# Performance work log

Measured on AMD Instinct MI355X. Metric: run time of the kernel, lower is better.

## Reference

```python
import jax, jax.numpy as jnp
import numpy as np

B, S, D = 4, 2048, 1024
NH, NKV = 16, 4
DK = D // NH          # 64
NG = NH // NKV        # 4


def _rope_tables(seq, d_k):
    theta = 1.0 / jnp.power(10000.0, jnp.arange(0, d_k, 2, dtype=jnp.float32) / d_k)
    ang = jnp.outer(jnp.arange(seq, dtype=jnp.float32), theta)  # [S, DK/2]
    ang = jnp.concatenate([ang, ang], axis=-1)                   # [S, DK]
    return jnp.cos(ang), jnp.sin(ang)


def _rotate_half(t):
    half = t.shape[-1] // 2
    return jnp.concatenate([-t[..., half:], t[..., :half]], axis=-1)


def _apply_rope(t, cos, sin):
    # t: [B, H, S, DK]; cos/sin: [S, DK]
    return t * cos + _rotate_half(t) * sin


def setup_inputs() -> dict:
    key = jax.random.key(0)
    ks = jax.random.split(key, 5)
    sc = 0.02
    x = jax.random.normal(ks[0], (B, S, D), dtype=jnp.float32)
    Wq = jax.random.normal(ks[1], (D, NH * DK), dtype=jnp.float32) * sc
    Wk = jax.random.normal(ks[2], (D, NKV * DK), dtype=jnp.float32) * sc
    Wv = jax.random.normal(ks[3], (D, NKV * DK), dtype=jnp.float32) * sc
    Wo = jax.random.normal(ks[4], (D, D), dtype=jnp.float32) * sc
    mask = jnp.tril(jnp.ones((S, S), dtype=bool))[None, None]  # causal [1,1,S,S]
    return {"x": x, "Wq": Wq, "Wk": Wk, "Wv": Wv, "Wo": Wo, "mask": mask}


def reference(x, Wq, Wk, Wv, Wo, mask):
    batch, seq, _ = x.shape
    q = (x @ Wq).reshape(batch, seq, NH, DK).transpose(0, 2, 1, 3)    # [B,NH,S,DK]
    k = (x @ Wk).reshape(batch, seq, NKV, DK).transpose(0, 2, 1, 3)   # [B,NKV,S,DK]
    v = (x @ Wv).reshape(batch, seq, NKV, DK).transpose(0, 2, 1, 3)

    cos, sin = _rope_tables(seq, DK)
    q = _apply_rope(q, cos, sin)
    k = _apply_rope(k, cos, sin)

    # GQA: repeat_interleave K/V along head dim
    k = jnp.repeat(k, NG, axis=1)  # [B,NH,S,DK]
    v = jnp.repeat(v, NG, axis=1)

    scores = jnp.einsum('bhqd,bhkd->bhqk', q, k) / jnp.sqrt(jnp.float32(DK))
    scores = jnp.where(mask, scores, jnp.float32(-jnp.inf))
    weights = jax.nn.softmax(scores, axis=-1)
    out = jnp.einsum('bhqk,bhkd->bhqd', weights, v)          # [B,NH,S,DK]
    out = out.transpose(0, 2, 1, 3).reshape(batch, seq, D)   # [B,S,D]
    return out @ Wo
```

## Files before the change

### kernel.cpp

```cpp
#include <hip/hip_runtime.h>

#define DEV __device__ __forceinline__

typedef short s16x8 __attribute__((ext_vector_type(8)));
typedef float f32x4 __attribute__((ext_vector_type(4)));


DEV unsigned short f2bf(float f) {
  union { float f; unsigned int u; } a; a.f = f;
  unsigned int u = a.u;
  u = (u + 0x7FFFu + ((u >> 16) & 1u)) >> 16;
  return (unsigned short)u;
}

DEV unsigned int bfpack2(float a, float b) {
  union { float f; unsigned int u; } x, y; x.f = a; y.f = b;
  return ((x.u + 0x8000u) >> 16) | ((y.u + 0x8000u) & 0xFFFF0000u);
}

DEV void gl_lds16(const void* g, void* l) {
  __builtin_amdgcn_global_load_lds(
      (const __attribute__((address_space(1))) unsigned int*)g,
      (__attribute__((address_space(3))) unsigned int*)l, 16, 0, 0);
}

__global__ __launch_bounds__(256) void cvt_kern(const float* __restrict__ src,
                                                unsigned short* __restrict__ dst) {
  int i = blockIdx.x * 256 + threadIdx.x;
  float4 v = ((const float4*)src)[i];
  ushort4 o = make_ushort4(f2bf(v.x), f2bf(v.y), f2bf(v.z), f2bf(v.w));
  ((ushort4*)dst)[i] = o;
}

__global__ __launch_bounds__(256) void transp_kern(const float* __restrict__ src,
                                                   unsigned short* __restrict__ dst,
                                                   int src_cols, int dst_off) {
  __shared__ float tile[32][33];
  int k0 = blockIdx.x * 32, n0 = blockIdx.y * 32;
  int tx = threadIdx.x & 31, ty = threadIdx.x >> 5;
  #pragma unroll
  for (int i = ty; i < 32; i += 8)
    tile[i][tx] = src[(k0 + i) * src_cols + (n0 + tx)];
  __syncthreads();
  #pragma unroll
  for (int i = ty; i < 32; i += 8)
    dst[(size_t)(n0 + i + dst_off) * 1024 + (k0 + tx)] = f2bf(tile[tx][i]);
}

template <int EPI>
__global__ __launch_bounds__(256) void gemm128(
    const unsigned short* __restrict__ A,
    const unsigned short* __restrict__ BT,
    unsigned short* __restrict__ Qbuf,
    unsigned short* __restrict__ Kbuf,
    unsigned short* __restrict__ VTbuf,
    float* __restrict__ Cout) {
  __shared__ __align__(16) unsigned short As[128 * 32];
  __shared__ __align__(16) unsigned short Bs[128 * 32];
  const int K = 1024;
  int m0 = blockIdx.x * 128, n0 = blockIdx.y * 128;
  int tid = threadIdx.x, w = tid >> 6, lane = tid & 63;
  int c4 = lane & 15, quad = lane >> 4;
  int m_off = (w & 1) * 64, n_off = (w >> 1) * 64;

  f32x4 acc[4][4];
  #pragma unroll
  for (int i = 0; i < 4; i++)
    #pragma unroll
    for (int j = 0; j < 4; j++) acc[i][j] = (f32x4){0.f, 0.f, 0.f, 0.f};

  int srow = (lane >> 2), sch = lane & 3;
  for (int kt = 0; kt < K / 32; ++kt) {
    int k0 = kt * 32;
    __syncthreads();
    #pragma unroll
    for (int ii = 0; ii < 2; ++ii) {
      int is = w * 2 + ii;
      int row = is * 16 + srow;
      gl_lds16(A + (size_t)(m0 + row) * K + k0 + sch * 8,
               (char*)As + is * 1024 + lane * 16);
      gl_lds16(BT + (size_t)(n0 + row) * K + k0 + sch * 8,
               (char*)Bs + is * 1024 + lane * 16);
    }
    __syncthreads();
    s16x8 a[4], b[4];
    #pragma unroll
    for (int mi = 0; mi < 4; ++mi)
      a[mi] = *(const s16x8*)((const char*)As + (m_off + mi * 16 + c4) * 64 + quad * 16);
    #pragma unroll
    for (int ni = 0; ni < 4; ++ni)
      b[ni] = *(const s16x8*)((const char*)Bs + (n_off + ni * 16 + c4) * 64 + quad * 16);
    #pragma unroll
    for (int mi = 0; mi < 4; ++mi)
      #pragma unroll
      for (int ni = 0; ni < 4; ++ni)
        acc[mi][ni] = __builtin_amdgcn_mfma_f32_16x16x32_bf16(a[mi], b[ni], acc[mi][ni], 0, 0, 0);
  }

  if (EPI == 1) {
    #pragma unroll
    for (int mi = 0; mi < 4; ++mi)
      #pragma unroll
      for (int ni = 0; ni < 4; ++ni)
        #pragma unroll
        for (int r = 0; r < 4; ++r) {
          int row = m0 + m_off + mi * 16 + quad * 4 + r;
          int col = n0 + n_off + ni * 16 + c4;
          Cout[(size_t)row * 1024 + col] = acc[mi][ni][r];
        }
  } else {
    int colbase = n0 + n_off;
    if (colbase < 1280) {
      const float CTH = 0.41524101186092029f;
      const float SC = 0.18033688011112042f;
      float th0 = exp2f(-(float)c4 * CTH);
      float th1 = exp2f(-(float)(c4 + 16) * CTH);
      bool isQ = colbase < 1024;
      float osc = isQ ? SC : 1.0f;
      #pragma unroll
      for (int mi = 0; mi < 4; ++mi)
        #pragma unroll
        for (int r = 0; r < 4; ++r) {
          int row = m0 + m_off + mi * 16 + quad * 4 + r;
          float pos = (float)(row & 2047);
          float a0 = pos * th0, a1 = pos * th1;
          float c0 = __cosf(a0), s0 = __sinf(a0);
          float c1 = __cosf(a1), s1 = __sinf(a1);
          float v0 = acc[mi][0][r], v1 = acc[mi][1][r];
          float v2 = acc[mi][2][r], v3 = acc[mi][3][r];
          float o0 = (v0 * c0 - v2 * s0) * osc;
          float o1 = (v1 * c1 - v3 * s1) * osc;
          float o2 = (v2 * c0 + v0 * s0) * osc;
          float o3 = (v3 * c1 + v1 * s1) * osc;
          if (isQ) {
            size_t base = (size_t)row * 1024 + colbase + c4;
            Qbuf[base] = f2bf(o0); Qbuf[base + 16] = f2bf(o1);
            Qbuf[base + 32] = f2bf(o2); Qbuf[base + 48] = f2bf(o3);
          } else {
            size_t base = (size_t)row * 256 + (colbase - 1024) + c4;
            Kbuf[base] = f2bf(o0); Kbuf[base + 16] = f2bf(o1);
            Kbuf[base + 32] = f2bf(o2); Kbuf[base + 48] = f2bf(o3);
          }
        }
    } else {
      #pragma unroll
      for (int mi = 0; mi < 4; ++mi)
        #pragma unroll
        for (int ni = 0; ni < 4; ++ni) {
          int row = m0 + m_off + mi * 16 + quad * 4;
          int c = colbase + ni * 16 + c4 - 1280;
          int bb = row >> 11, s = row & 2047;
          uint2 pv = make_uint2(bfpack2(acc[mi][ni][0], acc[mi][ni][1]),
                                bfpack2(acc[mi][ni][2], acc[mi][ni][3]));
          *(uint2*)(VTbuf + ((size_t)(bb * 256 + c)) * 2048 + s) = pv;
        }
    }
  }
}

__global__ __launch_bounds__(256, 4) void attn_kern(
    const unsigned short* __restrict__ Qbuf,
    const unsigned short* __restrict__ Kbuf,
    const unsigned short* __restrict__ VTbuf,
    unsigned short* __restrict__ Obuf) {
  __shared__ __align__(16) unsigned short Ks[2][64 * 64];
  __shared__ __align__(16) unsigned short VTs[2][64 * 64];
  __shared__ __align__(16) unsigned short Ps[4 * 16 * 64];

  int pr = blockIdx.x;
  int h = blockIdx.y, b = blockIdx.z, g = h >> 2;
  int tid = threadIdx.x, w = tid >> 6, lane = tid & 63;
  int c4 = lane & 15, quad = lane >> 4;
  int x7 = c4 & 7;
  unsigned short* Pw = Ps + w * 1024;

  int L0 = tid, L1 = tid + 256;
  int r0 = L0 >> 3, c0 = (L0 & 7) ^ (r0 & 7);
  int r1 = L1 >> 3, c1 = (L1 & 7) ^ (r1 & 7);
  const unsigned short* kB0 = Kbuf + (size_t)(b * 2048 + r0) * 256 + g * 64 + c0 * 8;
  const unsigned short* kB1 = Kbuf + (size_t)(b * 2048 + r1) * 256 + g * 64 + c1 * 8;
  const unsigned short* vB0 = VTbuf + (size_t)(b * 256 + g * 64 + r0) * 2048 + c0 * 8;
  const unsigned short* vB1 = VTbuf + (size_t)(b * 256 + g * 64 + r1) * 2048 + c1 * 8;

  for (int ph = 0; ph < 2; ++ph) {
    int qtile = ph ? (31 - pr) : pr;
    int nkv = qtile + 1;
    int q0 = qtile * 64;

    s16x8 bq[2];
    #pragma unroll
    for (int kk = 0; kk < 2; ++kk)
      bq[kk] = *(const s16x8*)(Qbuf +
          (size_t)(b * 2048 + q0 + w * 16 + c4) * 1024 + h * 64 + kk * 32 + quad * 8);

    const unsigned short* kS0 = kB0;
    const unsigned short* kS1 = kB1;
    const unsigned short* vS0 = vB0;
    const unsigned short* vS1 = vB1;

    f32x4 Oacc[4];
    #pragma unroll
    for (int nd = 0; nd < 4; ++nd) Oacc[nd] = (f32x4){0.f, 0.f, 0.f, 0.f};
    float m_st = -3e38f, l_st = 0.f;

    __syncthreads();
    gl_lds16(kS0, (char*)Ks[0] + L0 * 16);
    gl_lds16(kS1, (char*)Ks[0] + L1 * 16);
    gl_lds16(vS0, (char*)VTs[0] + L0 * 16);
    gl_lds16(vS1, (char*)VTs[0] + L1 * 16);
    kS0 += 64 * 256; kS1 += 64 * 256; vS0 += 64; vS1 += 64;

    for (int kt = 0; kt < nkv; ++kt) {
      int cur = kt & 1, nxt = cur ^ 1;
      __syncthreads();

      if (kt + 1 < nkv) {
        gl_lds16(kS0, (char*)Ks[nxt] + L0 * 16);
        gl_lds16(kS1, (char*)Ks[nxt] + L1 * 16);
        gl_lds16(vS0, (char*)VTs[nxt] + L0 * 16);
        gl_lds16(vS1, (char*)VTs[nxt] + L1 * 16);
        kS0 += 64 * 256; kS1 += 64 * 256; vS0 += 64; vS1 += 64;
      }

      const char* Kc = (const char*)Ks[cur];
      const char* Vc = (const char*)VTs[cur];

      f32x4 st[4];
      #pragma unroll
      for (int mt = 0; mt < 4; ++mt) st[mt] = (f32x4){0.f, 0.f, 0.f, 0.f};
      #pragma unroll
      for (int kk = 0; kk < 2; ++kk) {
        #pragma unroll
        for (int mt = 0; mt < 4; ++mt) {
          s16x8 ak = *(const s16x8*)(Kc + (mt * 16 + c4) * 128 +
                                     ((kk * 4 + quad) ^ x7) * 16);
          st[mt] = __builtin_amdgcn_mfma_f32_16x16x32_bf16(ak, bq[kk], st[mt], 0, 0, 0);
        }
      }

      int qmin = q0 + w * 16;
      if (kt * 64 + 63 > qmin) {
        int qi = qmin + c4;
        #pragma unroll
        for (int mt = 0; mt < 4; ++mt)
          #pragma unroll
          for (int r = 0; r < 4; ++r) {
            int kv = kt * 64 + mt * 16 + quad * 4 + r;
            if (kv > qi) st[mt][r] = -1e30f;
          }
      }

      float x0 = fmaxf(fmaxf(st[0][0], st[0][1]), fmaxf(st[0][2], st[0][3]));
      float x1 = fmaxf(fmaxf(st[1][0], st[1][1]), fmaxf(st[1][2], st[1][3]));
      float x2 = fmaxf(fmaxf(st[2][0], st[2][1]), fmaxf(st[2][2], st[2][3]));
      float x3 = fmaxf(fmaxf(st[3][0], st[3][1]), fmaxf(st[3][2], st[3][3]));
      float vmax = fmaxf(fmaxf(x0, x1), fmaxf(x2, x3));
      vmax = fmaxf(vmax, __shfl_xor(vmax, 16));
      vmax = fmaxf(vmax, __shfl_xor(vmax, 32));
      float mnew = fmaxf(m_st, vmax);
      float alpha = exp2f(m_st - mnew);
      m_st = mnew;

      #pragma unroll
      for (int mt = 0; mt < 4; ++mt)
        #pragma unroll
        for (int r = 0; r < 4; ++r) st[mt][r] = exp2f(st[mt][r] - mnew);
      float p0 = (st[0][0] + st[0][1]) + (st[0][2] + st[0][3]);
      float p1 = (st[1][0] + st[1][1]) + (st[1][2] + st[1][3]);
      float p2 = (st[2][0] + st[2][1]) + (st[2][2] + st[2][3]);
      float p3 = (st[3][0] + st[3][1]) + (st[3][2] + st[3][3]);
      float ssum = (p0 + p1) + (p2 + p3);
      ssum += __shfl_xor(ssum, 16);
      ssum += __shfl_xor(ssum, 32);
      l_st = l_st * alpha + ssum;

      #pragma unroll
      for (int nd = 0; nd < 4; ++nd)
        #pragma unroll
        for (int r = 0; r < 4; ++r) Oacc[nd][r] *= alpha;

      #pragma unroll
      for (int mt = 0; mt < 4; ++mt) {
        unsigned int lo = bfpack2(st[mt][0], st[mt][1]);
        unsigned int hi = bfpack2(st[mt][2], st[mt][3]);
        int cc = (mt * 2 + (quad >> 1)) ^ x7;
        *(uint2*)((char*)Pw + c4 * 128 + cc * 16 + (quad & 1) * 8) =
            make_uint2(lo, hi);
      }

      #pragma unroll
      for (int kk = 0; kk < 2; ++kk) {
        s16x8 ap = *(const s16x8*)((const char*)Pw + c4 * 128 +
                                   ((kk * 4 + quad) ^ x7) * 16);
        #pragma unroll
        for (int nd = 0; nd < 4; ++nd) {
          s16x8 av = *(const s16x8*)(Vc + (nd * 16 + c4) * 128 +
                                     ((kk * 4 + quad) ^ x7) * 16);
          Oacc[nd] = __builtin_amdgcn_mfma_f32_16x16x32_bf16(av, ap, Oacc[nd], 0, 0, 0);
        }
      }
    }

    float linv = 1.f / l_st;
    #pragma unroll
    for (int nd = 0; nd < 4; ++nd) {
      unsigned int lo = bfpack2(Oacc[nd][0] * linv, Oacc[nd][1] * linv);
      unsigned int hi = bfpack2(Oacc[nd][2] * linv, Oacc[nd][3] * linv);
      int cc = (nd * 2 + (quad >> 1)) ^ x7;
      *(uint2*)((char*)Pw + c4 * 128 + cc * 16 + (quad & 1) * 8) =
          make_uint2(lo, hi);
    }
    {
      int row = lane >> 2, j = lane & 3;
      int grow = b * 2048 + q0 + w * 16 + row;
      #pragma unroll
      for (int t = 0; t < 2; ++t) {
        int cb = j * 2 + t;
        uint4 v = *(const uint4*)((const char*)Pw + row * 128 +
                                  (cb ^ (row & 7)) * 16);
        *(uint4*)(Obuf + (size_t)grow * 1024 + h * 64 + cb * 8) = v;
      }
    }
  }
}

extern "C" void kernel_launch(void* const* d_in, const int* in_sizes, int n_in,
                              void* d_out, int out_size, void* d_ws, size_t ws_size,
                              hipStream_t stream) {
  const float* x  = (const float*)d_in[0];
  const float* Wq = (const float*)d_in[1];
  const float* Wk = (const float*)d_in[2];
  const float* Wv = (const float*)d_in[3];
  const float* Wo = (const float*)d_in[4];
  float* out = (float*)d_out;

  unsigned short* xb    = (unsigned short*)d_ws;
  unsigned short* WqkvT = xb + 8192 * 1024;
  unsigned short* WoT   = WqkvT + 1536 * 1024;
  unsigned short* Qbuf  = WoT + 1024 * 1024;
  unsigned short* Kbuf  = Qbuf + 8192 * 1024;
  unsigned short* VTbuf = Kbuf + 8192 * 256;
  unsigned short* Obuf  = VTbuf + 4 * 256 * 2048;

  cvt_kern<<<8192, 256, 0, stream>>>(x, xb);
  transp_kern<<<dim3(32, 32), 256, 0, stream>>>(Wq, WqkvT, 1024, 0);
  transp_kern<<<dim3(32, 8), 256, 0, stream>>>(Wk, WqkvT, 256, 1024);
  transp_kern<<<dim3(32, 8), 256, 0, stream>>>(Wv, WqkvT, 256, 1280);
  transp_kern<<<dim3(32, 32), 256, 0, stream>>>(Wo, WoT, 1024, 0);

  gemm128<0><<<dim3(64, 12), 256, 0, stream>>>(xb, WqkvT, Qbuf, Kbuf, VTbuf, nullptr);
  attn_kern<<<dim3(16, 16, 4), 256, 0, stream>>>(Qbuf, Kbuf, VTbuf, Obuf);
  gemm128<1><<<dim3(64, 8), 256, 0, stream>>>(Obuf, WoT, nullptr, nullptr, nullptr, out);
}
```

Baseline: 274.3 us.

## Widen GEMM K-tile to 64 with XOR-swizzled LDS, merge QKV transposes, truncate P

The bf16 GEMM now stages 64-wide K tiles into LDS with an XOR swizzle on 16-byte chunks. This halves the number of barrier-separated load iterations and is meant to avoid LDS bank conflicts on the fragment reads. The three Q/K/V weight transposes are merged into one launch. In attention, the probability packing switches from rounding to a single byte-permute truncation, trading a little precision for fewer ALU ops. LDS use doubles per GEMM block, which could reduce occupancy.

```diff
diff --git a/kernel.cpp b/kernel.cpp
--- a/kernel.cpp
+++ b/kernel.cpp
@@ -16,6 +16,11 @@
 DEV unsigned int bfpack2(float a, float b) {
   union { float f; unsigned int u; } x, y; x.f = a; y.f = b;
   return ((x.u + 0x8000u) >> 16) | ((y.u + 0x8000u) & 0xFFFF0000u);
+}
+
+DEV unsigned int pktrunc(float a, float b) {
+  union { float f; unsigned int u; } x, y; x.f = a; y.f = b;
+  return __builtin_amdgcn_perm(y.u, x.u, 0x07060302u);
 }
 
 DEV void gl_lds16(const void* g, void* l) {
@@ -45,6 +50,26 @@
   #pragma unroll
   for (int i = ty; i < 32; i += 8)
     dst[(size_t)(n0 + i + dst_off) * 1024 + (k0 + tx)] = f2bf(tile[tx][i]);
+}
+
+__global__ __launch_bounds__(256) void transp_qkv(const float* __restrict__ Wq,
+                                                  const float* __restrict__ Wk,
+                                                  const float* __restrict__ Wv,
+                                                  unsigned short* __restrict__ dst) {
+  __shared__ float tile[32][33];
+  int k0 = blockIdx.x * 32, n0 = blockIdx.y * 32;
+  const float* src; int sc, nloc;
+  if (n0 < 1024)      { src = Wq; sc = 1024; nloc = n0; }
+  else if (n0 < 1280) { src = Wk; sc = 256;  nloc = n0 - 1024; }
+  else                { src = Wv; sc = 256;  nloc = n0 - 1280; }
+  int tx = threadIdx.x & 31, ty = threadIdx.x >> 5;
+  #pragma unroll
+  for (int i = ty; i < 32; i += 8)
+    tile[i][tx] = src[(k0 + i) * sc + (nloc + tx)];
+  __syncthreads();
+  #pragma unroll
+  for (int i = ty; i < 32; i += 8)
+    dst[(size_t)(n0 + i) * 1024 + (k0 + tx)] = f2bf(tile[tx][i]);
 }
 
 template <int EPI>
@@ -55,12 +80,13 @@
     unsigned short* __restrict__ Kbuf,
     unsigned short* __restrict__ VTbuf,
     float* __restrict__ Cout) {
-  __shared__ __align__(16) unsigned short As[128 * 32];
-  __shared__ __align__(16) unsigned short Bs[128 * 32];
+  __shared__ __align__(16) unsigned short As[128 * 64];
+  __shared__ __align__(16) unsigned short Bs[128 * 64];
   const int K = 1024;
   int m0 = blockIdx.x * 128, n0 = blockIdx.y * 128;
   int tid = threadIdx.x, w = tid >> 6, lane = tid & 63;
   int c4 = lane & 15, quad = lane >> 4;
+  int x7 = c4 & 7;
   int m_off = (w & 1) * 64, n_off = (w >> 1) * 64;
 
   f32x4 acc[4][4];
@@ -69,32 +95,42 @@
     #pragma unroll
     for (int j = 0; j < 4; j++) acc[i][j] = (f32x4){0.f, 0.f, 0.f, 0.f};
 
-  int srow = (lane >> 2), sch = lane & 3;
-  for (int kt = 0; kt < K / 32; ++kt) {
-    int k0 = kt * 32;
+  const unsigned short* pA[4];
+  const unsigned short* pB[4];
+  #pragma unroll
+  for (int i = 0; i < 4; ++i) {
+    int slot = i * 256 + tid;
+    int row = slot >> 3, cs = slot & 7, lc = cs ^ (row & 7);
+    pA[i] = A + (size_t)(m0 + row) * K + lc * 8;
+    pB[i] = BT + (size_t)(n0 + row) * K + lc * 8;
+  }
+
+  for (int kt = 0; kt < K / 64; ++kt) {
     __syncthreads();
     #pragma unroll
-    for (int ii = 0; ii < 2; ++ii) {
-      int is = w * 2 + ii;
-      int row = is * 16 + srow;
-      gl_lds16(A + (size_t)(m0 + row) * K + k0 + sch * 8,
-               (char*)As + is * 1024 + lane * 16);
-      gl_lds16(BT + (size_t)(n0 + row) * K + k0 + sch * 8,
-               (char*)Bs + is * 1024 + lane * 16);
+    for (int i = 0; i < 4; ++i) {
+      int slot = i * 256 + tid;
+      gl_lds16(pA[i], (char*)As + slot * 16);
+      gl_lds16(pB[i], (char*)Bs + slot * 16);
+      pA[i] += 64; pB[i] += 64;
     }
     __syncthreads();
-    s16x8 a[4], b[4];
-    #pragma unroll
-    for (int mi = 0; mi < 4; ++mi)
-      a[mi] = *(const s16x8*)((const char*)As + (m_off + mi * 16 + c4) * 64 + quad * 16);
-    #pragma unroll
-    for (int ni = 0; ni < 4; ++ni)
-      b[ni] = *(const s16x8*)((const char*)Bs + (n_off + ni * 16 + c4) * 64 + quad * 16);
-    #pragma unroll
-    for (int mi = 0; mi < 4; ++mi)
+    #pragma unroll
+    for (int kk = 0; kk < 2; ++kk) {
+      s16x8 a[4], b[4];
+      int cc = ((kk * 4 + quad) ^ x7) * 16;
+      #pragma unroll
+      for (int mi = 0; mi < 4; ++mi)
+        a[mi] = *(const s16x8*)((const char*)As + (m_off + mi * 16 + c4) * 128 + cc);
       #pragma unroll
       for (int ni = 0; ni < 4; ++ni)
-        acc[mi][ni] = __builtin_amdgcn_mfma_f32_16x16x32_bf16(a[mi], b[ni], acc[mi][ni], 0, 0, 0);
+        b[ni] = *(const s16x8*)((const char*)Bs + (n_off + ni * 16 + c4) * 128 + cc);
+      #pragma unroll
+      for (int mi = 0; mi < 4; ++mi)
+        #pragma unroll
+        for (int ni = 0; ni < 4; ++ni)
+          acc[mi][ni] = __builtin_amdgcn_mfma_f32_16x16x32_bf16(a[mi], b[ni], acc[mi][ni], 0, 0, 0);
+    }
   }
 
   if (EPI == 1) {
@@ -281,8 +317,8 @@
 
       #pragma unroll
       for (int mt = 0; mt < 4; ++mt) {
-        unsigned int lo = bfpack2(st[mt][0], st[mt][1]);
-        unsigned int hi = bfpack2(st[mt][2], st[mt][3]);
+        unsigned int lo = pktrunc(st[mt][0], st[mt][1]);
+        unsigned int hi = pktrunc(st[mt][2], st[mt][3]);
         int cc = (mt * 2 + (quad >> 1)) ^ x7;
         *(uint2*)((char*)Pw + c4 * 128 + cc * 16 + (quad & 1) * 8) =
             make_uint2(lo, hi);
@@ -343,9 +379,7 @@
   unsigned short* Obuf  = VTbuf + 4 * 256 * 2048;
 
   cvt_kern<<<8192, 256, 0, stream>>>(x, xb);
-  transp_kern<<<dim3(32, 32), 256, 0, stream>>>(Wq, WqkvT, 1024, 0);
-  transp_kern<<<dim3(32, 8), 256, 0, stream>>>(Wk, WqkvT, 256, 1024);
-  transp_kern<<<dim3(32, 8), 256, 0, stream>>>(Wv, WqkvT, 256, 1280);
+  transp_qkv<<<dim3(32, 48), 256, 0, stream>>>(Wq, Wk, Wv, WqkvT);
   transp_kern<<<dim3(32, 32), 256, 0, stream>>>(Wo, WoT, 1024, 0);
 
   gemm128<0><<<dim3(64, 12), 256, 0, stream>>>(xb, WqkvT, Qbuf, Kbuf, VTbuf, nullptr);
```

Result: faster. 249.6 us (-9.0%).
